# Optimization experiments

Measured on AMD Instinct MI355X. Metric: run time of the kernel, lower is better.

The kernel has to match this reference:

```python
import jax, jax.numpy as jnp
import numpy as np

DIM_CODES = 512
DICT_SIZE = 512
EMBED_DIM = 16
BATCH = 512


def setup_inputs() -> dict:
    key = jax.random.key(0)
    k1, k2 = jax.random.split(key)
    mu = jax.random.normal(k1, (BATCH, DIM_CODES * EMBED_DIM), dtype=jnp.float32)
    dictionary = jax.random.normal(k2, (DIM_CODES, DICT_SIZE, EMBED_DIM), dtype=jnp.float32)
    return {"mu": mu, "dictionary": dictionary}


def reference(mu, dictionary):
    # mu: [B, C*E], dictionary: [C, K, E]
    B = mu.shape[0]
    C, K, E = dictionary.shape
    mu3 = mu.reshape(B, C, E)
    # pairwise squared distance ||mu - d||^2 = ||mu||^2 + ||d||^2 - 2 mu.d -> [B, C, K]
    dist = (jnp.sum(mu3 * mu3, axis=-1)[..., None]
            + jnp.sum(dictionary * dictionary, axis=-1)[None]
            - 2.0 * jnp.einsum('bce,cke->bck', mu3, dictionary))
    idx = jnp.argmin(dist, axis=-1)  # [B, C] int
    # gather nearest codebook entries: per-code index into its own codebook
    z_embed = dictionary[jnp.arange(C)[None, :], idx]  # [B, C, E]
    z_embed = z_embed.reshape(B, C * E)
    # TransferGrad: forward = z_embed, backward passes grad straight-through to mu
    z = mu + jax.lax.stop_gradient(z_embed - mu)
    one_hot_idx = jax.nn.one_hot(idx, K, dtype=mu.dtype)  # [B, C, K]
    return z, z_embed, one_hot_idx
```

## Files before the change

### kernel.cpp

```cpp
#include <hip/hip_runtime.h>
#include <float.h>

constexpr int C    = 512;
constexpr int K    = 512;
constexpr int E    = 16;
constexpr int B    = 512;
constexpr int RB   = 256;
constexpr int MUS  = C * E;

__launch_bounds__(256, 4)
__global__ void vq_kernel(const float* __restrict__ mu,
                          const float* __restrict__ dict,
                          float* __restrict__ z,
                          float* __restrict__ zq,
                          float* __restrict__ oh)
{
    const int c    = blockIdx.x;
    const int b0   = blockIdx.y * RB;
    const int tid  = threadIdx.x;
    const int lane = tid & 63;
    const int wave = tid >> 6;

    __shared__ __align__(16) float dict_s[K * E];
    __shared__ float nrm_s[K];

    const float* __restrict__ dbase = dict + (size_t)c * K * E;

#pragma unroll
    for (int rep = 0; rep < 2; ++rep) {
        const int k = tid + rep * 256;
        const float4* p = reinterpret_cast<const float4*>(dbase + k * E);
        const float4 d0 = p[0], d1 = p[1], d2 = p[2], d3 = p[3];
        float s = d0.x * d0.x;
        s = fmaf(d0.y, d0.y, s); s = fmaf(d0.z, d0.z, s); s = fmaf(d0.w, d0.w, s);
        s = fmaf(d1.x, d1.x, s); s = fmaf(d1.y, d1.y, s);
        s = fmaf(d1.z, d1.z, s); s = fmaf(d1.w, d1.w, s);
        s = fmaf(d2.x, d2.x, s); s = fmaf(d2.y, d2.y, s);
        s = fmaf(d2.z, d2.z, s); s = fmaf(d2.w, d2.w, s);
        s = fmaf(d3.x, d3.x, s); s = fmaf(d3.y, d3.y, s);
        s = fmaf(d3.z, d3.z, s); s = fmaf(d3.w, d3.w, s);
        float4* q4 = reinterpret_cast<float4*>(&dict_s[k * E]);
        q4[0] = d0; q4[1] = d1; q4[2] = d2; q4[3] = d3;
        nrm_s[k] = s;
    }
    __syncthreads();

    const int myrow = (wave << 6) + lane;
    const float* __restrict__ mrow = mu + (size_t)(b0 + myrow) * MUS + c * E;
    float4 m0, m1, m2, m3;
    {
        const float4* p = reinterpret_cast<const float4*>(mrow);
        m0 = p[0]; m1 = p[1]; m2 = p[2]; m3 = p[3];
    }
    float nm = m0.x * m0.x;
    nm = fmaf(m0.y, m0.y, nm); nm = fmaf(m0.z, m0.z, nm); nm = fmaf(m0.w, m0.w, nm);
    nm = fmaf(m1.x, m1.x, nm); nm = fmaf(m1.y, m1.y, nm);
    nm = fmaf(m1.z, m1.z, nm); nm = fmaf(m1.w, m1.w, nm);
    nm = fmaf(m2.x, m2.x, nm); nm = fmaf(m2.y, m2.y, nm);
    nm = fmaf(m2.z, m2.z, nm); nm = fmaf(m2.w, m2.w, nm);
    nm = fmaf(m3.x, m3.x, nm); nm = fmaf(m3.y, m3.y, nm);
    nm = fmaf(m3.z, m3.z, nm); nm = fmaf(m3.w, m3.w, nm);

    float bd = FLT_MAX, sec = FLT_MAX;
    int   bk = K;
    const float4* __restrict__ ds4 = reinterpret_cast<const float4*>(dict_s);
#pragma unroll 4
    for (int k = 0; k < K; ++k) {
        const float4 d0 = ds4[k * 4 + 0];
        const float4 d1 = ds4[k * 4 + 1];
        const float4 d2 = ds4[k * 4 + 2];
        const float4 d3 = ds4[k * 4 + 3];
        float acc = d0.x * m0.x;
        acc = fmaf(d0.y, m0.y, acc); acc = fmaf(d0.z, m0.z, acc); acc = fmaf(d0.w, m0.w, acc);
        acc = fmaf(d1.x, m1.x, acc); acc = fmaf(d1.y, m1.y, acc);
        acc = fmaf(d1.z, m1.z, acc); acc = fmaf(d1.w, m1.w, acc);
        acc = fmaf(d2.x, m2.x, acc); acc = fmaf(d2.y, m2.y, acc);
        acc = fmaf(d2.z, m2.z, acc); acc = fmaf(d2.w, m2.w, acc);
        acc = fmaf(d3.x, m3.x, acc); acc = fmaf(d3.y, m3.y, acc);
        acc = fmaf(d3.z, m3.z, acc); acc = fmaf(d3.w, m3.w, acc);
        const float dist = fmaf(-2.0f, acc, nm + nrm_s[k]);
        const bool  lt   = dist < bd;
        sec = lt ? bd : fminf(sec, dist);
        bd  = lt ? dist : bd;
        bk  = lt ? k : bk;
    }

    unsigned long long trig = __ballot(sec < bd + 1e-3f);
    while (trig) {
        const int r = __ffsll(trig) - 1;
        trig &= trig - 1;
        const int row = (wave << 6) + r;
        const float* __restrict__ qrow = mu + (size_t)(b0 + row) * MUS + c * E;

        double nmuD = 0.0;
#pragma unroll
        for (int t = 0; t < E; ++t) {
            const double mt = (double)qrow[t];
            nmuD += mt * mt;
        }
        double bD = DBL_MAX;
        int    bK = K;
#pragma unroll
        for (int i = 0; i < 8; ++i) {
            const int k = lane + 64 * i;
            const float* dk = &dict_s[k * E];
            double nd = 0.0, dt = 0.0;
#pragma unroll
            for (int t = 0; t < 4; ++t) {
                const double dx = dk[4 * t + 0], dy = dk[4 * t + 1];
                const double dz = dk[4 * t + 2], dw = dk[4 * t + 3];
                const double mx = qrow[4 * t + 0], my = qrow[4 * t + 1];
                const double mz = qrow[4 * t + 2], mw = qrow[4 * t + 3];
                nd += dx * dx + dy * dy + dz * dz + dw * dw;
                dt += dx * mx + dy * my + dz * mz + dw * mw;
            }
            const double dist = nmuD + nd - 2.0 * dt;
            if (dist < bD) { bD = dist; bK = k; }
        }
#pragma unroll
        for (int off = 32; off; off >>= 1) {
            const double od = __shfl_down(bD, off);
            const int    ok = __shfl_down(bK, off);
            if (od < bD || (od == bD && ok < bK)) { bD = od; bK = ok; }
        }
        const int kwin = __shfl(bK, 0);
        if (lane == r) bk = kwin;
    }

#pragma unroll 4
    for (int r = 0; r < 64; ++r) {
        const int kk  = __shfl(bk, r);
        const int row = (wave << 6) + r;
        const int b   = b0 + row;

        float* ohp = oh + ((size_t)b * C + c) * K;
#pragma unroll
        for (int h = 0; h < 2; ++h) {
            const int kb = h * 256 + lane * 4;
            float4 v;
            v.x = (kb + 0 == kk) ? 1.0f : 0.0f;
            v.y = (kb + 1 == kk) ? 1.0f : 0.0f;
            v.z = (kb + 2 == kk) ? 1.0f : 0.0f;
            v.w = (kb + 3 == kk) ? 1.0f : 0.0f;
            *reinterpret_cast<float4*>(ohp + kb) = v;
        }

        if (lane < E) {
            const float dq = dict_s[kk * E + lane];
            const float mm = mu[(size_t)b * MUS + (size_t)c * E + lane];
            const size_t o = (size_t)b * MUS + (size_t)c * E + lane;
            zq[o] = dq;
            z[o]  = mm + (dq - mm);
        }
    }
}

extern "C" void kernel_launch(void* const* d_in, const int* in_sizes, int n_in,
                              void* d_out, int out_size, void* d_ws, size_t ws_size,
                              hipStream_t stream)
{
    const float* mu   = (const float*)d_in[0];
    const float* dict = (const float*)d_in[1];

    float* z  = (float*)d_out;
    float* zq = z  + (size_t)B * C * E;
    float* oh = zq + (size_t)B * C * E;

    dim3 grid(C, B / RB);
    vq_kernel<<<grid, 256, 0, stream>>>(mu, dict, z, zq, oh);
}
```

Measured before the change: 701.5 us.

## Split one-hot writing into separate streaming kernel with nontemporal stores

```diff
diff --git a/kernel.cpp b/kernel.cpp
--- a/kernel.cpp
+++ b/kernel.cpp
@@ -8,12 +8,14 @@
 constexpr int RB   = 256;
 constexpr int MUS  = C * E;
 
+typedef float f32x4 __attribute__((ext_vector_type(4)));
+
 __launch_bounds__(256, 4)
-__global__ void vq_kernel(const float* __restrict__ mu,
-                          const float* __restrict__ dict,
-                          float* __restrict__ z,
-                          float* __restrict__ zq,
-                          float* __restrict__ oh)
+__global__ void vq_scan(const float* __restrict__ mu,
+                        const float* __restrict__ dict,
+                        float* __restrict__ z,
+                        float* __restrict__ zq,
+                        int*   __restrict__ idx_t)
 {
     const int c    = blockIdx.x;
     const int b0   = blockIdx.y * RB;
@@ -46,7 +48,8 @@
     __syncthreads();
 
     const int myrow = (wave << 6) + lane;
-    const float* __restrict__ mrow = mu + (size_t)(b0 + myrow) * MUS + c * E;
+    const int b     = b0 + myrow;
+    const float* __restrict__ mrow = mu + (size_t)b * MUS + c * E;
     float4 m0, m1, m2, m3;
     {
         const float4* p = reinterpret_cast<const float4*>(mrow);
@@ -127,31 +130,53 @@
         if (lane == r) bk = kwin;
     }
 
+    idx_t[c * B + b] = bk;
+
+    {
+        const float4* dwin = reinterpret_cast<const float4*>(&dict_s[bk * E]);
+        const float4 q0 = dwin[0], q1 = dwin[1], q2 = dwin[2], q3 = dwin[3];
+        float* zqp = zq + (size_t)b * MUS + (size_t)c * E;
+        float* zp  = z  + (size_t)b * MUS + (size_t)c * E;
+        reinterpret_cast<float4*>(zqp)[0] = q0;
+        reinterpret_cast<float4*>(zqp)[1] = q1;
+        reinterpret_cast<float4*>(zqp)[2] = q2;
+        reinterpret_cast<float4*>(zqp)[3] = q3;
+        float4 z0, z1, z2, z3;
+        z0.x = m0.x + (q0.x - m0.x); z0.y = m0.y + (q0.y - m0.y);
+        z0.z = m0.z + (q0.z - m0.z); z0.w = m0.w + (q0.w - m0.w);
+        z1.x = m1.x + (q1.x - m1.x); z1.y = m1.y + (q1.y - m1.y);
+        z1.z = m1.z + (q1.z - m1.z); z1.w = m1.w + (q1.w - m1.w);
+        z2.x = m2.x + (q2.x - m2.x); z2.y = m2.y + (q2.y - m2.y);
+        z2.z = m2.z + (q2.z - m2.z); z2.w = m2.w + (q2.w - m2.w);
+        z3.x = m3.x + (q3.x - m3.x); z3.y = m3.y + (q3.y - m3.y);
+        z3.z = m3.z + (q3.z - m3.z); z3.w = m3.w + (q3.w - m3.w);
+        reinterpret_cast<float4*>(zp)[0] = z0;
+        reinterpret_cast<float4*>(zp)[1] = z1;
+        reinterpret_cast<float4*>(zp)[2] = z2;
+        reinterpret_cast<float4*>(zp)[3] = z3;
+    }
+}
+
+__launch_bounds__(256)
+__global__ void vq_onehot(const int* __restrict__ idx_t,
+                          float* __restrict__ oh)
+{
+    const long TOT = (long)B * C * K / 4;
+    const long stride = (long)gridDim.x * blockDim.x;
+    long f4 = (long)blockIdx.x * blockDim.x + threadIdx.x;
 #pragma unroll 4
-    for (int r = 0; r < 64; ++r) {
-        const int kk  = __shfl(bk, r);
-        const int row = (wave << 6) + r;
-        const int b   = b0 + row;
-
-        float* ohp = oh + ((size_t)b * C + c) * K;
-#pragma unroll
-        for (int h = 0; h < 2; ++h) {
-            const int kb = h * 256 + lane * 4;
-            float4 v;
-            v.x = (kb + 0 == kk) ? 1.0f : 0.0f;
-            v.y = (kb + 1 == kk) ? 1.0f : 0.0f;
-            v.z = (kb + 2 == kk) ? 1.0f : 0.0f;
-            v.w = (kb + 3 == kk) ? 1.0f : 0.0f;
-            *reinterpret_cast<float4*>(ohp + kb) = v;
-        }
-
-        if (lane < E) {
-            const float dq = dict_s[kk * E + lane];
-            const float mm = mu[(size_t)b * MUS + (size_t)c * E + lane];
-            const size_t o = (size_t)b * MUS + (size_t)c * E + lane;
-            zq[o] = dq;
-            z[o]  = mm + (dq - mm);
-        }
+    for (; f4 < TOT; f4 += stride) {
+        const int rowu = __builtin_amdgcn_readfirstlane((int)(f4 >> 7));
+        const int bb   = rowu >> 9;
+        const int cc   = rowu & (C - 1);
+        const int kk   = idx_t[cc * B + bb];
+        const int k0   = ((int)f4 & 127) << 2;
+        f32x4 v;
+        v.x = (k0 + 0 == kk) ? 1.0f : 0.0f;
+        v.y = (k0 + 1 == kk) ? 1.0f : 0.0f;
+        v.z = (k0 + 2 == kk) ? 1.0f : 0.0f;
+        v.w = (k0 + 3 == kk) ? 1.0f : 0.0f;
+        __builtin_nontemporal_store(v, reinterpret_cast<f32x4*>(oh) + f4);
     }
 }
 
@@ -166,6 +191,9 @@
     float* zq = z  + (size_t)B * C * E;
     float* oh = zq + (size_t)B * C * E;
 
-    dim3 grid(C, B / RB);
-    vq_kernel<<<grid, 256, 0, stream>>>(mu, dict, z, zq, oh);
+    int* idx_t = (int*)d_ws;
+
+    dim3 g1(C, B / RB);
+    vq_scan<<<g1, 256, 0, stream>>>(mu, dict, z, zq, idx_t);
+    vq_onehot<<<2048, 256, 0, stream>>>(idx_t, oh);
 }
```

New measurement: 701.6 us. About the same (+0.0%).
